# Performance work log

Measured on AMD Instinct MI355X. Metric: run time of the kernel, lower is better.

Reference implementation:

```python
import jax, jax.numpy as jnp
import numpy as np

OBS_DIM = 32
STATE_DIM = 5
LSTM_H = 64
T_HID = 128
O_HID = 128
B = 128
T = 2048


def _xavier(key, shape):
    fan_out, fan_in = shape
    std = (2.0 / (fan_in + fan_out)) ** 0.5
    return jax.random.normal(key, shape, dtype=jnp.float32) * std


def setup_inputs() -> dict:
    key = jax.random.key(0)
    ks = jax.random.split(key, 16)
    inp = {}
    inp["observations"] = jax.random.normal(ks[0], (B, T, OBS_DIM), dtype=jnp.float32)
    # LSTM params (PyTorch layout: [4H, in], gate order i,f,g,o)
    inp["lstm_Wih"] = _xavier(ks[1], (4 * LSTM_H, OBS_DIM))
    inp["lstm_Whh"] = _xavier(ks[2], (4 * LSTM_H, LSTM_H))
    inp["lstm_bih"] = jnp.zeros((4 * LSTM_H,), dtype=jnp.float32)
    inp["lstm_bhh"] = jnp.zeros((4 * LSTM_H,), dtype=jnp.float32)
    # transition MLP
    inp["t_w1"] = _xavier(ks[3], (T_HID, LSTM_H + STATE_DIM))
    inp["t_b1"] = jnp.zeros((T_HID,), dtype=jnp.float32)
    inp["t_g"] = jnp.ones((T_HID,), dtype=jnp.float32)
    inp["t_beta"] = jnp.zeros((T_HID,), dtype=jnp.float32)
    inp["t_w2"] = _xavier(ks[4], (T_HID // 2, T_HID))
    inp["t_b2"] = jnp.zeros((T_HID // 2,), dtype=jnp.float32)
    inp["t_w3"] = _xavier(ks[5], (2 * STATE_DIM, T_HID // 2))
    inp["t_b3"] = jnp.zeros((2 * STATE_DIM,), dtype=jnp.float32)
    # observation MLP
    inp["o_w1"] = _xavier(ks[6], (O_HID, STATE_DIM))
    inp["o_b1"] = jnp.zeros((O_HID,), dtype=jnp.float32)
    inp["o_g"] = jnp.ones((O_HID,), dtype=jnp.float32)
    inp["o_beta"] = jnp.zeros((O_HID,), dtype=jnp.float32)
    inp["o_w2"] = _xavier(ks[7], (O_HID // 2, O_HID))
    inp["o_b2"] = jnp.zeros((O_HID // 2,), dtype=jnp.float32)
    inp["o_w3"] = _xavier(ks[8], (2 * OBS_DIM, O_HID // 2))
    inp["o_b3"] = jnp.zeros((2 * OBS_DIM,), dtype=jnp.float32)
    inp["z0_mean"] = jnp.zeros((STATE_DIM,), dtype=jnp.float32)
    inp["z0_log_var"] = jnp.zeros((STATE_DIM,), dtype=jnp.float32)
    return inp


def _layernorm(x, g, b, eps=1e-5):
    m = jnp.mean(x, axis=-1, keepdims=True)
    v = jnp.mean((x - m) ** 2, axis=-1, keepdims=True)
    return (x - m) * jax.lax.rsqrt(v + eps) * g + b


def _forward(observations, lstm_Wih, lstm_Whh, lstm_bih, lstm_bhh,
             t_w1, t_b1, t_g, t_beta, t_w2, t_b2, t_w3, t_b3,
             o_w1, o_b1, o_g, o_beta, o_w2, o_b2, o_w3, o_b3,
             z0_mean, z0_log_var):
    b, s, _ = observations.shape
    # ---- LSTM (batch_first); precompute input projection, scan over time ----
    x_proj = jnp.einsum("bti,gi->btg", observations, lstm_Wih) + lstm_bih + lstm_bhh  # [B,T,4H]
    x_proj = jnp.swapaxes(x_proj, 0, 1)  # [T,B,4H]

    def lstm_step(carry, xt):
        h, c = carry
        gates = xt + h @ lstm_Whh.T
        i, f, g, o = jnp.split(gates, 4, axis=-1)
        i = jax.nn.sigmoid(i); f = jax.nn.sigmoid(f)
        g = jnp.tanh(g); o = jax.nn.sigmoid(o)
        c = f * c + i * g
        h = o * jnp.tanh(c)
        return (h, c), h

    h0 = jnp.zeros((b, LSTM_H), dtype=observations.dtype)
    c0 = jnp.zeros((b, LSTM_H), dtype=observations.dtype)
    _, lstm_seq = jax.lax.scan(lstm_step, (h0, c0), x_proj)  # [T,B,H]

    # ---- state-space recurrence (eval mode: z = transition mean) ----
    z0 = jnp.broadcast_to(z0_mean, (b, STATE_DIM))

    def trans_step(z, lstm_t):
        comb = jnp.concatenate([lstm_t, z], axis=-1)            # [B, H+S]
        h1 = jnp.tanh(_layernorm(comb @ t_w1.T + t_b1, t_g, t_beta))
        h2 = jnp.tanh(h1 @ t_w2.T + t_b2)
        out = h2 @ t_w3.T + t_b3                                 # [B, 2S]
        mean = out[..., :STATE_DIM]
        log_var = jnp.clip(out[..., STATE_DIM:], -10.0, 10.0)
        return mean, (mean, log_var)

    _, (t_means, t_lvs) = jax.lax.scan(trans_step, z0, lstm_seq[1:])  # [T-1,B,S]

    trans_means = jnp.concatenate([z0[None], t_means], axis=0)                              # [T,B,S]
    trans_log_vars = jnp.concatenate([jnp.broadcast_to(z0_log_var, (1, b, STATE_DIM)), t_lvs], axis=0)
    states = trans_means  # eval mode: z_t == trans_mean_t, z_0 == z0_mean

    # ---- observation head, vectorized over all timesteps ----
    h1 = jnp.tanh(_layernorm(states @ o_w1.T + o_b1, o_g, o_beta))
    h2 = jnp.tanh(h1 @ o_w2.T + o_b2)
    out = h2 @ o_w3.T + o_b3                                      # [T,B,2*obs_dim]
    obs_means = out[..., :OBS_DIM]
    obs_log_vars = jnp.clip(out[..., OBS_DIM:], -10.0, 10.0)

    # move to batch_first [B,T,*]
    return (jnp.swapaxes(obs_means, 0, 1),
            jnp.swapaxes(obs_log_vars, 0, 1),
            jnp.swapaxes(trans_means, 0, 1),
            jnp.swapaxes(trans_log_vars, 0, 1))


def reference(observations, lstm_Wih, lstm_Whh, lstm_bih, lstm_bhh,
              t_w1, t_b1, t_g, t_beta, t_w2, t_b2, t_w3, t_b3,
              o_w1, o_b1, o_g, o_beta, o_w2, o_b2, o_w3, o_b3,
              z0_mean, z0_log_var):
    return _forward(observations, lstm_Wih, lstm_Whh, lstm_bih, lstm_bhh,
                    t_w1, t_b1, t_g, t_beta, t_w2, t_b2, t_w3, t_b3,
                    o_w1, o_b1, o_g, o_beta, o_w2, o_b2, o_w3, o_b3,
                    z0_mean, z0_log_var)
```

## Files before the change

kernel.cpp:

```cpp
#include <hip/hip_runtime.h>

#define B_ 128
#define T_ 2048

typedef float vf32 __attribute__((ext_vector_type(32)));

__device__ __forceinline__ float fast_sigmoid(float x){
    return 1.0f / (1.0f + __expf(-x));
}
__device__ __forceinline__ float fast_tanh(float x){
    float a = fabsf(x);
    float e = __expf(2.0f*a);
    float r = 1.0f - 2.0f/(e + 1.0f);
    return (x < 0.0f) ? -r : r;
}

template<int CTRL>
__device__ __forceinline__ float dpp_mov(float x){
    return __int_as_float(__builtin_amdgcn_update_dpp(
        0, __float_as_int(x), CTRL, 0xF, 0xF, true));
}

__device__ __forceinline__ float wave_sum64(float v){
    v += dpp_mov<0xB1>(v);
    v += dpp_mov<0x4E>(v);
    v += dpp_mov<0x141>(v);
    v += dpp_mov<0x140>(v);
#if __has_builtin(__builtin_amdgcn_permlane16_swap)
    {
        auto r = __builtin_amdgcn_permlane16_swap(__float_as_int(v),
                                                  __float_as_int(v), false, false);
        v = __int_as_float(r[0]) + __int_as_float(r[1]);
    }
#else
    v += __shfl_xor(v, 16, 64);
#endif
#if __has_builtin(__builtin_amdgcn_permlane32_swap)
    {
        auto r = __builtin_amdgcn_permlane32_swap(__float_as_int(v),
                                                  __float_as_int(v), false, false);
        v = __int_as_float(r[0]) + __int_as_float(r[1]);
    }
#else
    v += __shfl_xor(v, 32, 64);
#endif
    return v;
}

__device__ __forceinline__ void wait_ge(int* p, int v){
    while (__hip_atomic_load(p, __ATOMIC_ACQUIRE, __HIP_MEMORY_SCOPE_WORKGROUP) < v) { }
}
__device__ __forceinline__ void st_rel(int* p, int v){
    __hip_atomic_store(p, v, __ATOMIC_RELEASE, __HIP_MEMORY_SCOPE_WORKGROUP);
}

__global__ __launch_bounds__(512)
__attribute__((amdgpu_waves_per_eu(2, 2)))
void scan_kernel(
    const float* __restrict__ obs,
    const float* __restrict__ Wih,
    const float* __restrict__ Whh,
    const float* __restrict__ bih,
    const float* __restrict__ bhh,
    const float* __restrict__ tw1,
    const float* __restrict__ tb1,
    const float* __restrict__ tg,
    const float* __restrict__ tbeta,
    const float* __restrict__ tw2,
    const float* __restrict__ tb2,
    const float* __restrict__ tw3,
    const float* __restrict__ tb3,
    const float* __restrict__ z0m,
    const float* __restrict__ z0lv,
    float* __restrict__ out_tm,
    float* __restrict__ out_tlv)
{
    __shared__ __align__(16) float hring[8][64];
    __shared__ __align__(16) float oring[8][32];
    __shared__ __align__(16) float A1ring[8][128];
    __shared__ __align__(16) float h1w[2][64];
    __shared__ float p2s[2][2][64];
    __shared__ int hflag[4];
    __shared__ int aflag[2];
    __shared__ int pf[2];
    __shared__ int ttag;

    const int tid  = threadIdx.x;
    const int wid  = tid >> 6;
    const int lane = tid & 63;
    const int b    = blockIdx.x;

    vf32 V0, V1, V2;
    #pragma unroll
    for (int k = 0; k < 32; k++) { V0[k]=0.f; V1[k]=0.f; V2[k]=0.f; }

    float biasg = 0.f, b1r = 0.f, gr = 0.f, betar = 0.f, b2r = 0.f, b3r = 0.f;
    float c_st = 0.f, carry = 0.f;

    if (wid < 4) {
        const int g  = lane & 3;
        const int uu = wid*16 + (lane >> 2);
        const int row = g*64 + uu;
        biasg = bih[row] + bhh[row];
        #pragma unroll
        for (int k = 0; k < 32; k++) V0[k] = Wih[row*32 + k];
        #pragma unroll
        for (int k = 0; k < 32; k++) V1[k] = Whh[row*64 + k];
        #pragma unroll
        for (int k = 0; k < 32; k++) V2[k] = Whh[row*64 + 32 + k];
        if (g == 1 && uu < 32) carry = obs[((size_t)b*T_ + 4)*32 + uu];
    } else if (wid < 6) {
        const int ks = wid - 4;
        #pragma unroll
        for (int k = 0; k < 32; k++) V0[k] = tw2[lane*128 + ks*64 + k];
        #pragma unroll
        for (int k = 0; k < 32; k++) V1[k] = tw2[lane*128 + ks*64 + 32 + k];
        #pragma unroll
        for (int k = 0; k < 5; k++) {
            V2[k]     = tw1[lane*69 + 64 + k];
            V2[5 + k] = tw1[(64 + lane)*69 + 64 + k];
        }
        const int r = ks*64 + lane;
        gr = tg[r]; betar = tbeta[r];
        b2r = tb2[lane];
        if (lane < 40) {
            #pragma unroll
            for (int k = 0; k < 16; k++)
                V2[10 + k] = tw3[(lane>>2)*64 + (lane&3)*16 + k];
            b3r = tb3[lane >> 2];
        }
    } else {
        const int r = (wid - 6)*64 + lane;
        #pragma unroll
        for (int k = 0; k < 32; k++) V0[k] = tw1[r*69 + k];
        #pragma unroll
        for (int k = 0; k < 32; k++) V1[k] = tw1[r*69 + 32 + k];
        b1r = tb1[r];
    }

    if (tid < 64) hring[7][tid] = 0.f;
    if (tid < 128) oring[tid >> 5][tid & 31] = obs[(size_t)b*T_*32 + tid];
    if (tid < 5) {
        out_tm [(size_t)b*T_*5 + tid] = z0m[tid];
        out_tlv[(size_t)b*T_*5 + tid] = z0lv[tid];
    }
    if (tid < 4) hflag[tid] = -1;
    if (tid < 2) { aflag[tid] = 0; pf[tid] = 0; }
    if (tid == 0) ttag = 0;
    __syncthreads();

    if (wid < 4) {
        const int g  = lane & 3;
        const int uu = wid*16 + (lane >> 2);
        for (int t = 0; t < T_; ++t) {
            wait_ge(&hflag[0], t-1); wait_ge(&hflag[1], t-1);
            wait_ge(&hflag[2], t-1); wait_ge(&hflag[3], t-1);
            wait_ge(&aflag[0], t-8); wait_ge(&aflag[1], t-8);

            const float4* ob = (const float4*)oring[t & 7];
            const float4* hp = (const float4*)hring[(t - 1) & 7];
            float a0 = biasg, a1 = 0.f, a2 = 0.f, a3 = 0.f;
            #pragma unroll
            for (int k4 = 0; k4 < 8; k4++) {
                float4 o = ob[k4];
                a0 += V0[k4*4+0]*o.x;
                a1 += V0[k4*4+1]*o.y;
                a2 += V0[k4*4+2]*o.z;
                a3 += V0[k4*4+3]*o.w;
            }
            #pragma unroll
            for (int k4 = 0; k4 < 8; k4++) {
                float4 h = hp[k4];
                a0 += V1[k4*4+0]*h.x;
                a1 += V1[k4*4+1]*h.y;
                a2 += V1[k4*4+2]*h.z;
                a3 += V1[k4*4+3]*h.w;
            }
            #pragma unroll
            for (int k4 = 0; k4 < 8; k4++) {
                float4 h = hp[8 + k4];
                a0 += V2[k4*4+0]*h.x;
                a1 += V2[k4*4+1]*h.y;
                a2 += V2[k4*4+2]*h.z;
                a3 += V2[k4*4+3]*h.w;
            }
            const float G = (a0 + a1) + (a2 + a3);

            const float x1 = dpp_mov<0xB1>(G);
            const float x2 = dpp_mov<0x4E>(G);
            const float x3 = dpp_mov<0x1B>(G);
            const bool c1 = (g & 1), c2 = (g & 2);
            float iv = c2 ? (c1 ? x3 : x2) : (c1 ? x1 : G );
            float fv = c2 ? (c1 ? x2 : x3) : (c1 ? G  : x1);
            float gv = c2 ? (c1 ? x1 : G ) : (c1 ? x3 : x2);
            float ov = c2 ? (c1 ? G  : x1) : (c1 ? x2 : x3);

            iv = fast_sigmoid(iv);
            fv = fast_sigmoid(fv);
            gv = fast_tanh(gv);
            ov = fast_sigmoid(ov);
            c_st = fv*c_st + iv*gv;
            const float hv = ov * fast_tanh(c_st);

            if (g == 0) hring[t & 7][uu] = hv;
            if (g == 1 && uu < 32 && t + 4 < T_) oring[(t + 4) & 7][uu] = carry;
            st_rel(&hflag[wid], t);
            if (g == 1 && uu < 32 && t + 5 < T_)
                carry = obs[((size_t)b*T_ + t + 5)*32 + uu];
        }
    } else if (wid < 6) {
        const int ks = wid - 4;
        float zr0 = z0m[0], zr1 = z0m[1], zr2 = z0m[2],
              zr3 = z0m[3], zr4 = z0m[4];
        for (int t = 1; t < T_; ++t) {
            wait_ge(&aflag[0], t); wait_ge(&aflag[1], t);

            float a0 = A1ring[t & 7][lane]
                     + V2[0]*zr0 + V2[1]*zr1 + V2[2]*zr2 + V2[3]*zr3 + V2[4]*zr4;
            float a1 = A1ring[t & 7][64 + lane]
                     + V2[5]*zr0 + V2[6]*zr1 + V2[7]*zr2 + V2[8]*zr3 + V2[9]*zr4;
            const float s1 = wave_sum64(a0 + a1);
            const float s2 = wave_sum64(a0*a0 + a1*a1);
            const float mean = s1 * (1.0f/128.0f);
            const float var  = fmaxf(s2 * (1.0f/128.0f) - mean*mean, 0.0f);
            const float rs   = rsqrtf(var + 1e-5f);
            const float aown = ks ? a1 : a0;
            const float h1v  = fast_tanh((aown - mean)*rs*gr + betar);

            h1w[ks][lane] = h1v;
            __builtin_amdgcn_wave_barrier();

            float p0 = 0.f, p1 = 0.f, p2 = 0.f, p3 = 0.f;
            const float4* h4 = (const float4*)h1w[ks];
            #pragma unroll
            for (int k4 = 0; k4 < 8; k4++) {
                float4 h = h4[k4];
                p0 += V0[k4*4+0]*h.x;
                p1 += V0[k4*4+1]*h.y;
                p2 += V0[k4*4+2]*h.z;
                p3 += V0[k4*4+3]*h.w;
            }
            #pragma unroll
            for (int k4 = 0; k4 < 8; k4++) {
                float4 h = h4[8 + k4];
                p0 += V1[k4*4+0]*h.x;
                p1 += V1[k4*4+1]*h.y;
                p2 += V1[k4*4+2]*h.z;
                p3 += V1[k4*4+3]*h.w;
            }
            const float p = (p0 + p1) + (p2 + p3);

            p2s[t & 1][ks][lane] = p;
            st_rel(&pf[ks], t);
            wait_ge(&pf[ks ^ 1], t);
            const float pother = p2s[t & 1][ks ^ 1][lane];

            const float h2v = fast_tanh(b2r + p + pother);
            const int pp = lane & 3;
            float ac0 = 0.f, ac1 = 0.f, ac2 = 0.f, ac3 = 0.f;
            #pragma unroll
            for (int k = 0; k < 4; k++) {
                ac0 += V2[10 + k]      * __shfl(h2v, pp*16 + k,      64);
                ac1 += V2[10 + 4 + k]  * __shfl(h2v, pp*16 + 4 + k,  64);
                ac2 += V2[10 + 8 + k]  * __shfl(h2v, pp*16 + 8 + k,  64);
                ac3 += V2[10 + 12 + k] * __shfl(h2v, pp*16 + 12 + k, 64);
            }
            float acc = (ac0 + ac1) + (ac2 + ac3);
            acc += dpp_mov<0xB1>(acc);
            acc += dpp_mov<0x4E>(acc);
            const float val = b3r + acc;

            if (ks == 0) {
                if (pp == 0 && lane < 40) {
                    const int j = lane >> 2;
                    const size_t row = (size_t)b*T_ + t;
                    if (j < 5) out_tm[row*5 + j] = val;
                    else out_tlv[row*5 + (j - 5)] =
                             fminf(10.0f, fmaxf(-10.0f, val));
                }
                st_rel(&ttag, t);
            }
            zr0 = __shfl(val, 0, 64);
            zr1 = __shfl(val, 4, 64);
            zr2 = __shfl(val, 8, 64);
            zr3 = __shfl(val, 12, 64);
            zr4 = __shfl(val, 16, 64);
        }
    } else {
        const int r = (wid - 6)*64 + lane;
        for (int t = 1; t < T_; ++t) {
            wait_ge(&hflag[0], t); wait_ge(&hflag[1], t);
            wait_ge(&hflag[2], t); wait_ge(&hflag[3], t);
            wait_ge(&ttag, t - 8);

            const float4* hv4 = (const float4*)hring[t & 7];
            float s0 = b1r, s1 = 0.f, s2 = 0.f, s3 = 0.f;
            #pragma unroll
            for (int k4 = 0; k4 < 8; k4++) {
                float4 h = hv4[k4];
                s0 += V0[k4*4+0]*h.x;
                s1 += V0[k4*4+1]*h.y;
                s2 += V0[k4*4+2]*h.z;
                s3 += V0[k4*4+3]*h.w;
            }
            #pragma unroll
            for (int k4 = 0; k4 < 8; k4++) {
                float4 h = hv4[8 + k4];
                s0 += V1[k4*4+0]*h.x;
                s1 += V1[k4*4+1]*h.y;
                s2 += V1[k4*4+2]*h.z;
                s3 += V1[k4*4+3]*h.w;
            }
            A1ring[t & 7][r] = (s0 + s1) + (s2 + s3);
            st_rel(&aflag[wid - 6], t);
        }
    }
}

#define DEC_BLOCKS 512

__global__ __launch_bounds__(512) void dec_kernel(
    const float* __restrict__ ow1,
    const float* __restrict__ ob1,
    const float* __restrict__ og,
    const float* __restrict__ obeta,
    const float* __restrict__ ow2,
    const float* __restrict__ ob2,
    const float* __restrict__ ow3,
    const float* __restrict__ ob3,
    const float* __restrict__ tmeans,
    float* __restrict__ out_om,
    float* __restrict__ out_olv)
{
    __shared__ float w1s[640];
    __shared__ float b1s[128], gs[128], bes[128];
    __shared__ float w2s[8192];
    __shared__ float b2s[64];
    __shared__ float w3s[4096];
    __shared__ float b3s[64];
    __shared__ __align__(16) float h1s[8][128];
    __shared__ __align__(16) float h2s[8][64];

    const int tid = threadIdx.x;
    for (int idx = tid; idx < 640; idx += 512) w1s[idx] = ow1[idx];
    for (int idx = tid; idx < 128; idx += 512) {
        b1s[idx] = ob1[idx]; gs[idx] = og[idx]; bes[idx] = obeta[idx];
    }
    for (int idx = tid; idx < 8192; idx += 512) {
        int k = idx >> 6, j = idx & 63;
        w2s[idx] = ow2[j*128 + k];
    }
    for (int idx = tid; idx < 4096; idx += 512) {
        int k = idx >> 6, j = idx & 63;
        w3s[idx] = ow3[j*64 + k];
    }
    for (int idx = tid; idx < 64; idx += 512) { b2s[idx] = ob2[idx]; b3s[idx] = ob3[idx]; }
    __syncthreads();

    const int lane   = tid & 63;
    const int wv     = tid >> 6;
    const int gwave  = (blockIdx.x * 512 + tid) >> 6;
    const int nwaves = DEC_BLOCKS * 8;
    const int j0 = lane, j1 = lane + 64;

    for (int row = gwave; row < B_*T_; row += nwaves) {
        const float z0v = tmeans[(size_t)row*5 + 0];
        const float z1v = tmeans[(size_t)row*5 + 1];
        const float z2v = tmeans[(size_t)row*5 + 2];
        const float z3v = tmeans[(size_t)row*5 + 3];
        const float z4v = tmeans[(size_t)row*5 + 4];

        float a = b1s[j0] + w1s[j0*5+0]*z0v + w1s[j0*5+1]*z1v + w1s[j0*5+2]*z2v
                + w1s[j0*5+3]*z3v + w1s[j0*5+4]*z4v;
        float bb = b1s[j1] + w1s[j1*5+0]*z0v + w1s[j1*5+1]*z1v + w1s[j1*5+2]*z2v
                 + w1s[j1*5+3]*z3v + w1s[j1*5+4]*z4v;
        const float s1 = wave_sum64(a + bb);
        const float s2 = wave_sum64(a*a + bb*bb);
        const float mean = s1 * (1.0f/128.0f);
        const float var  = fmaxf(s2 * (1.0f/128.0f) - mean*mean, 0.0f);
        const float rs   = rsqrtf(var + 1e-5f);
        const float h1a  = fast_tanh((a  - mean)*rs*gs[j0] + bes[j0]);
        const float h1b  = fast_tanh((bb - mean)*rs*gs[j1] + bes[j1]);

        h1s[wv][lane]      = h1a;
        h1s[wv][64 + lane] = h1b;
        __builtin_amdgcn_wave_barrier();

        float acc2a = b2s[lane], acc2b = 0.f, acc2c = 0.f, acc2d = 0.f;
        const float4* h14 = (const float4*)(h1s[wv]);
        #pragma unroll
        for (int k4 = 0; k4 < 32; k4++) {
            float4 h = h14[k4];
            acc2a += h.x * w2s[(k4*4+0)*64 + lane];
            acc2b += h.y * w2s[(k4*4+1)*64 + lane];
            acc2c += h.z * w2s[(k4*4+2)*64 + lane];
            acc2d += h.w * w2s[(k4*4+3)*64 + lane];
        }
        const float h2v = fast_tanh(acc2a + acc2b + acc2c + acc2d);

        h2s[wv][lane] = h2v;
        __builtin_amdgcn_wave_barrier();

        float acc3a = b3s[lane], acc3b = 0.f, acc3c = 0.f, acc3d = 0.f;
        const float4* h24 = (const float4*)(h2s[wv]);
        #pragma unroll
        for (int k4 = 0; k4 < 16; k4++) {
            float4 h = h24[k4];
            acc3a += h.x * w3s[(k4*4+0)*64 + lane];
            acc3b += h.y * w3s[(k4*4+1)*64 + lane];
            acc3c += h.z * w3s[(k4*4+2)*64 + lane];
            acc3d += h.w * w3s[(k4*4+3)*64 + lane];
        }
        const float acc3 = acc3a + acc3b + acc3c + acc3d;

        if (lane < 32) {
            out_om[(size_t)row*32 + lane] = acc3;
        } else {
            out_olv[(size_t)row*32 + (lane - 32)] = fminf(10.0f, fmaxf(-10.0f, acc3));
        }
    }
}

extern "C" void kernel_launch(void* const* d_in, const int* in_sizes, int n_in,
                              void* d_out, int out_size, void* d_ws, size_t ws_size,
                              hipStream_t stream) {
    const float* obs  = (const float*)d_in[0];
    const float* Wih  = (const float*)d_in[1];
    const float* Whh  = (const float*)d_in[2];
    const float* bih  = (const float*)d_in[3];
    const float* bhh  = (const float*)d_in[4];
    const float* tw1  = (const float*)d_in[5];
    const float* tb1  = (const float*)d_in[6];
    const float* tg   = (const float*)d_in[7];
    const float* tbe  = (const float*)d_in[8];
    const float* tw2  = (const float*)d_in[9];
    const float* tb2  = (const float*)d_in[10];
    const float* tw3  = (const float*)d_in[11];
    const float* tb3  = (const float*)d_in[12];
    const float* ow1  = (const float*)d_in[13];
    const float* ob1  = (const float*)d_in[14];
    const float* og   = (const float*)d_in[15];
    const float* obe  = (const float*)d_in[16];
    const float* ow2  = (const float*)d_in[17];
    const float* ob2  = (const float*)d_in[18];
    const float* ow3  = (const float*)d_in[19];
    const float* ob3  = (const float*)d_in[20];
    const float* z0m  = (const float*)d_in[21];
    const float* z0lv = (const float*)d_in[22];

    float* out0 = (float*)d_out;
    float* out1 = out0 + (size_t)B_*T_*32;
    float* out2 = out1 + (size_t)B_*T_*32;
    float* out3 = out2 + (size_t)B_*T_*5;

    scan_kernel<<<B_, 512, 0, stream>>>(obs, Wih, Whh, bih, bhh,
                                        tw1, tb1, tg, tbe, tw2, tb2, tw3, tb3,
                                        z0m, z0lv, out2, out3);

    dec_kernel<<<DEC_BLOCKS, 512, 0, stream>>>(
        ow1, ob1, og, obe, ow2, ob2, ow3, ob3, out2, out0, out1);
}
```

Baseline: 2.759 ms.

## Consolidate inter-wave flags into atomic counter and chained flags with sleep polling

Replaces the four per-wave LSTM flags with one shared atomic counter that each LSTM wave increments once per step. The two A1 producer flags become a chain: wave 7 waits on wave 6 and then publishes a single flag. Waits on non-critical lag dependencies now poll with s_sleep, flag stores come from lane 0 only, and cross-lane broadcasts use readlane instead of shfl. The aim is fewer LDS polling loads and less contention on the serial per-timestep critical path. In exchange, the atomic increment and the extra a6→a7 hop may add latency to that same path.

```diff
diff --git a/kernel.cpp b/kernel.cpp
--- a/kernel.cpp
+++ b/kernel.cpp
@@ -47,8 +47,16 @@
     return v;
 }
 
+__device__ __forceinline__ float readlane_f(float v, int l){
+    return __int_as_float(__builtin_amdgcn_readlane(__float_as_int(v), l));
+}
+
 __device__ __forceinline__ void wait_ge(int* p, int v){
     while (__hip_atomic_load(p, __ATOMIC_ACQUIRE, __HIP_MEMORY_SCOPE_WORKGROUP) < v) { }
+}
+__device__ __forceinline__ void wait_ge_slp(int* p, int v){
+    while (__hip_atomic_load(p, __ATOMIC_ACQUIRE, __HIP_MEMORY_SCOPE_WORKGROUP) < v)
+        __builtin_amdgcn_s_sleep(1);
 }
 __device__ __forceinline__ void st_rel(int* p, int v){
     __hip_atomic_store(p, v, __ATOMIC_RELEASE, __HIP_MEMORY_SCOPE_WORKGROUP);
@@ -80,8 +88,8 @@
     __shared__ __align__(16) float A1ring[8][128];
     __shared__ __align__(16) float h1w[2][64];
     __shared__ float p2s[2][2][64];
-    __shared__ int hflag[4];
-    __shared__ int aflag[2];
+    __shared__ int hcnt;
+    __shared__ int a6, a7;
     __shared__ int pf[2];
     __shared__ int ttag;
 
@@ -144,18 +152,15 @@
         out_tm [(size_t)b*T_*5 + tid] = z0m[tid];
         out_tlv[(size_t)b*T_*5 + tid] = z0lv[tid];
     }
-    if (tid < 4) hflag[tid] = -1;
-    if (tid < 2) { aflag[tid] = 0; pf[tid] = 0; }
-    if (tid == 0) ttag = 0;
+    if (tid == 0) { hcnt = 0; a6 = 0; a7 = 0; pf[0] = 0; pf[1] = 0; ttag = 0; }
     __syncthreads();
 
     if (wid < 4) {
         const int g  = lane & 3;
         const int uu = wid*16 + (lane >> 2);
         for (int t = 0; t < T_; ++t) {
-            wait_ge(&hflag[0], t-1); wait_ge(&hflag[1], t-1);
-            wait_ge(&hflag[2], t-1); wait_ge(&hflag[3], t-1);
-            wait_ge(&aflag[0], t-8); wait_ge(&aflag[1], t-8);
+            wait_ge(&hcnt, 4*t);
+            wait_ge_slp(&a7, t - 8);
 
             const float4* ob = (const float4*)oring[t & 7];
             const float4* hp = (const float4*)hring[(t - 1) & 7];
@@ -204,7 +209,9 @@
 
             if (g == 0) hring[t & 7][uu] = hv;
             if (g == 1 && uu < 32 && t + 4 < T_) oring[(t + 4) & 7][uu] = carry;
-            st_rel(&hflag[wid], t);
+            if (lane == 0)
+                __hip_atomic_fetch_add(&hcnt, 1, __ATOMIC_RELEASE,
+                                       __HIP_MEMORY_SCOPE_WORKGROUP);
             if (g == 1 && uu < 32 && t + 5 < T_)
                 carry = obs[((size_t)b*T_ + t + 5)*32 + uu];
         }
@@ -213,7 +220,7 @@
         float zr0 = z0m[0], zr1 = z0m[1], zr2 = z0m[2],
               zr3 = z0m[3], zr4 = z0m[4];
         for (int t = 1; t < T_; ++t) {
-            wait_ge(&aflag[0], t); wait_ge(&aflag[1], t);
+            wait_ge(&a7, t);
 
             float a0 = A1ring[t & 7][lane]
                      + V2[0]*zr0 + V2[1]*zr1 + V2[2]*zr2 + V2[3]*zr3 + V2[4]*zr4;
@@ -251,7 +258,7 @@
             const float p = (p0 + p1) + (p2 + p3);
 
             p2s[t & 1][ks][lane] = p;
-            st_rel(&pf[ks], t);
+            if (lane == 0) st_rel(&pf[ks], t);
             wait_ge(&pf[ks ^ 1], t);
             const float pother = p2s[t & 1][ks ^ 1][lane];
 
@@ -278,20 +285,19 @@
                     else out_tlv[row*5 + (j - 5)] =
                              fminf(10.0f, fmaxf(-10.0f, val));
                 }
-                st_rel(&ttag, t);
-            }
-            zr0 = __shfl(val, 0, 64);
-            zr1 = __shfl(val, 4, 64);
-            zr2 = __shfl(val, 8, 64);
-            zr3 = __shfl(val, 12, 64);
-            zr4 = __shfl(val, 16, 64);
+                if (lane == 0) st_rel(&ttag, t);
+            }
+            zr0 = readlane_f(val, 0);
+            zr1 = readlane_f(val, 4);
+            zr2 = readlane_f(val, 8);
+            zr3 = readlane_f(val, 12);
+            zr4 = readlane_f(val, 16);
         }
     } else {
         const int r = (wid - 6)*64 + lane;
         for (int t = 1; t < T_; ++t) {
-            wait_ge(&hflag[0], t); wait_ge(&hflag[1], t);
-            wait_ge(&hflag[2], t); wait_ge(&hflag[3], t);
-            wait_ge(&ttag, t - 8);
+            wait_ge(&hcnt, 4*(t + 1));
+            wait_ge_slp(&ttag, t - 8);
 
             const float4* hv4 = (const float4*)hring[t & 7];
             float s0 = b1r, s1 = 0.f, s2 = 0.f, s3 = 0.f;
@@ -312,7 +318,12 @@
                 s3 += V1[k4*4+3]*h.w;
             }
             A1ring[t & 7][r] = (s0 + s1) + (s2 + s3);
-            st_rel(&aflag[wid - 6], t);
+            if (wid == 6) {
+                if (lane == 0) st_rel(&a6, t);
+            } else {
+                wait_ge(&a6, t);
+                if (lane == 0) st_rel(&a7, t);
+            }
         }
     }
 }
```

Result: no change. 2.754 ms (-0.2%).
